# Optimization experiments

Hardware: AMD Instinct MI355X
Metric: run time of the kernel (lower is better)

The kernel has to match this reference:

```python
import jax, jax.numpy as jnp
import numpy as np

B, L, T = 4, 512, 4096
HID, NH = 1024, 16
HD = HID // NH
MAX_POS = 4096
BASE = 10000.0


def _cos_sin(dim, max_pos, base):
    inv_freq = 1.0 / base ** (jnp.arange(0, dim, 2, dtype=jnp.float32) / dim)
    t = jnp.arange(max_pos, dtype=jnp.float32)
    freqs = jnp.einsum('i,j->ij', t, inv_freq)
    emb = jnp.concatenate([freqs, freqs], axis=-1)  # [max_pos, dim]
    return jnp.cos(emb), jnp.sin(emb)


def _rotate_half(x):
    x1, x2 = x[..., : x.shape[-1] // 2], x[..., x.shape[-1] // 2:]
    return jnp.concatenate([-x2, x1], axis=-1)


def setup_inputs() -> dict:
    key = jax.random.key(0)
    ks = jax.random.split(key, 12)
    s = 0.02
    inp = {
        'latents': jax.random.normal(ks[0], (B, L, HID), jnp.float32),
        'target': jax.random.normal(ks[1], (B, T, HID), jnp.float32),
        'target_mask': jax.random.randint(ks[2], (B, T), 0, 2).astype(bool),
        'target_timestamp': jnp.sort(jax.random.randint(ks[3], (B, T), 0, MAX_POS), axis=-1),
        'Wq': jax.random.normal(ks[4], (HID, HID), jnp.float32) * s,
        'bq': jnp.zeros((HID,), jnp.float32),
        'Wk': jax.random.normal(ks[5], (HID, HID), jnp.float32) * s,
        'bk': jnp.zeros((HID,), jnp.float32),
        'Wv': jax.random.normal(ks[6], (HID, HID), jnp.float32) * s,
        'bv': jnp.zeros((HID,), jnp.float32),
        'Wo': jax.random.normal(ks[7], (HID, HID), jnp.float32) * s,
        'bo': jnp.zeros((HID,), jnp.float32),
    }
    return inp


def reference(latents, target, target_mask, target_timestamp, Wq, bq, Wk, bk, Wv, bv, Wo, bo):
    cos, sin = _cos_sin(HD, MAX_POS, BASE)  # [MAX_POS, HD]
    # latents_timestamp: arange(L) * (max-1)/(L-1), cast to int
    lat_ts = (jnp.arange(L, dtype=jnp.float32) * (MAX_POS - 1) / (L - 1)).astype(jnp.int64)
    lat_ts = jnp.broadcast_to(lat_ts[None, :], (B, L))

    # QKV projections (torch Linear: x @ W.T + b)
    q = (latents @ Wq.T + bq).reshape(B, L, NH, HD).transpose(0, 2, 1, 3)  # [B,H,L,D]
    k = (target @ Wk.T + bk).reshape(B, T, NH, HD).transpose(0, 2, 1, 3)   # [B,H,T,D]
    v = (target @ Wv.T + bv).reshape(B, T, NH, HD).transpose(0, 2, 1, 3)

    # RoPE with gathered timestamps; unsqueeze over head dim
    cq, sq = cos[lat_ts][:, None], sin[lat_ts][:, None]          # [B,1,L,D]
    ck, sk = cos[target_timestamp][:, None], sin[target_timestamp][:, None]  # [B,1,T,D]
    q = q * cq + _rotate_half(q) * sq
    k = k * ck + _rotate_half(k) * sk

    # SDPA with boolean attn mask (True = attend)
    scores = jnp.einsum('bhld,bhtd->bhlt', q, k) / jnp.sqrt(jnp.float32(HD))
    bias = jnp.where(target_mask[:, None, None, :], 0.0, -jnp.inf).astype(scores.dtype)
    attn = jax.nn.softmax(scores + bias, axis=-1)
    out = jnp.einsum('bhlt,bhtd->bhld', attn, v)  # [B,H,L,D]
    out = out.transpose(0, 2, 1, 3).reshape(B, L, HID)
    return out @ Wo.T + bo
```

## Files before the change

kernel.cpp:

```cpp
#include <hip/hip_runtime.h>

#define B_ 4
#define L_ 512
#define T_ 4096
#define NH_ 16
#define HD_ 64

using f32x4 = __attribute__((ext_vector_type(4))) float;
using bf16x8 = __attribute__((ext_vector_type(8))) short;
using u32x4 = __attribute__((ext_vector_type(4))) unsigned int;

__device__ __forceinline__ unsigned short f2bf(float x) {
  unsigned int u = __builtin_bit_cast(unsigned int, x);
  u += 0x7fffu + ((u >> 16) & 1u);
  return (unsigned short)(u >> 16);
}

__device__ __forceinline__ unsigned cvtpk(float lo, float hi) {
  unsigned r;
  asm("v_cvt_pk_bf16_f32 %0, %1, %2" : "=v"(r) : "v"(lo), "v"(hi));
  return r;
}

__device__ __forceinline__ u32x4 cvt8(const float4& a, const float4& b) {
  u32x4 r;
  r[0] = (unsigned)f2bf(a.x) | ((unsigned)f2bf(a.y) << 16);
  r[1] = (unsigned)f2bf(a.z) | ((unsigned)f2bf(a.w) << 16);
  r[2] = (unsigned)f2bf(b.x) | ((unsigned)f2bf(b.y) << 16);
  r[3] = (unsigned)f2bf(b.z) | ((unsigned)f2bf(b.w) << 16);
  return r;
}

__device__ __forceinline__ void gload16(const void* g, void* l) {
  __builtin_amdgcn_global_load_lds(
      (const __attribute__((address_space(1))) unsigned int*)g,
      (__attribute__((address_space(3))) unsigned int*)l, 16, 0, 0);
}

#define BC8(x) __builtin_bit_cast(bf16x8, (x))

struct CvtArgs {
  const float* src[6];
  unsigned short* dst[6];
  int cum[7];
};

__global__ void cvt_bf16(CvtArgs a, int total) {
  for (int g = blockIdx.x * 256 + threadIdx.x; g < total; g += gridDim.x * 256) {
    int r = 0;
#pragma unroll
    for (int q = 0; q < 5; ++q) r += (g >= a.cum[q + 1]);
    const int lc = g - a.cum[r];
    const float4* s = (const float4*)a.src[r] + (size_t)lc * 2;
    float4 x0 = s[0], x1 = s[1];
    *((u32x4*)a.dst[r] + lc) = cvt8(x0, x1);
  }
}

__global__ void rope_table(float* __restrict__ cost, float* __restrict__ sint,
                           const int* __restrict__ mask, float* __restrict__ mbias) {
  const int idx = blockIdx.x * 256 + threadIdx.x;
  const int pos = idx >> 5, i = idx & 31;
  const float inv = 1.0f / powf(10000.0f, (float)(2 * i) * (1.0f / 64.0f));
  const float f = (float)pos * inv;
  cost[idx] = cosf(f);
  sint[idx] = sinf(f);
  if (idx < B_ * T_) mbias[idx] = mask[idx] ? 0.f : -1e30f;
}

template <int EPI>
__global__ __launch_bounds__(256, 2) void gemm_bf(
    const unsigned short* __restrict__ A, const unsigned short* __restrict__ Wb,
    const float* __restrict__ bias, void* __restrict__ outp,
    const float* __restrict__ cost, const float* __restrict__ sint,
    const int* __restrict__ ts) {
  __shared__ u32x4 lsA[2][512];
  __shared__ u32x4 lsB[2][512];
  const int tid = threadIdx.x;
  const int mt = blockIdx.x >> 3, nt = blockIdx.x & 7;
  const int mBase = mt << 7, nBase = nt << 7;
  const int lane = tid & 63, wid = tid >> 6;
  const int wr = wid >> 1, wc = wid & 1;
  const int lr = lane & 15, lg = lane >> 4;

  f32x4 acc[4][4];
#pragma unroll
  for (int m = 0; m < 4; ++m)
#pragma unroll
    for (int n = 0; n < 4; ++n) acc[m][n] = (f32x4){0.f, 0.f, 0.f, 0.f};

  auto stage = [&](int bi, int kt) {
    const int ko = kt * 32;
#pragma unroll
    for (int j2 = 0; j2 < 2; ++j2) {
      const int j = wid * 2 + j2;
      const int row = (j & 1) * 64 + lane;
      const int kg = j >> 1;
      gload16(A + (size_t)(mBase + row) * 1024 + ko + kg * 8,
              (unsigned short*)lsA[bi] + j * 512);
      gload16(Wb + (size_t)(nBase + row) * 1024 + ko + kg * 8,
              (unsigned short*)lsB[bi] + j * 512);
    }
  };

  stage(0, 0);
  __syncthreads();
  int cur = 0;
  for (int kt = 0; kt < 32; ++kt) {
    if (kt < 31) stage(cur ^ 1, kt + 1);
    const u32x4* As = lsA[cur];
    const u32x4* Bs = lsB[cur];
    bf16x8 af[4], bfr[4];
#pragma unroll
    for (int m = 0; m < 4; ++m) af[m] = BC8(As[lg * 128 + wr * 64 + m * 16 + lr]);
#pragma unroll
    for (int n = 0; n < 4; ++n) bfr[n] = BC8(Bs[lg * 128 + wc * 64 + n * 16 + lr]);
#pragma unroll
    for (int m = 0; m < 4; ++m)
#pragma unroll
      for (int n = 0; n < 4; ++n)
        acc[m][n] = __builtin_amdgcn_mfma_f32_16x16x32_bf16(af[m], bfr[n], acc[m][n], 0, 0, 0);
    __syncthreads();
    cur ^= 1;
  }

  float bv[4];
#pragma unroll
  for (int n = 0; n < 4; ++n) bv[n] = bias[nBase + wc * 64 + n * 16 + lr];

  if (EPI == 3) {
    float* Of = (float*)outp;
#pragma unroll
    for (int m = 0; m < 4; ++m)
#pragma unroll
      for (int r = 0; r < 4; ++r) {
        const int gR = mBase + wr * 64 + m * 16 + lg * 4 + r;
#pragma unroll
        for (int n = 0; n < 4; ++n)
          Of[(size_t)gR * 1024 + nBase + wc * 64 + n * 16 + lr] = acc[m][n][r] + bv[n];
      }
  } else {
    unsigned short* Qo = (unsigned short*)outp;
    const int h = (nBase >> 6) + wc;
#pragma unroll
    for (int m = 0; m < 4; ++m) {
#pragma unroll
      for (int r = 0; r < 4; ++r) {
        const int gR = mBase + wr * 64 + m * 16 + lg * 4 + r;
        const int b2 = gR >> 9, p2 = gR & 511;
        const int pos = (int)(((float)p2 * 4095.0f) / 511.0f);
        const float* cp = cost + pos * 32;
        const float* sp = sint + pos * 32;
        const size_t obase = (((size_t)(b2 * NH_ + h)) * L_ + p2) * HD_;
#pragma unroll
        for (int n = 0; n < 2; ++n) {
          const int d = n * 16 + lr;
          const float x1 = acc[m][n][r] + bv[n];
          const float x2 = acc[m][n + 2][r] + bv[n + 2];
          const float c = cp[d], s = sp[d];
          Qo[obase + d] = f2bf(x1 * c - x2 * s);
          Qo[obase + d + 32] = f2bf(x2 * c + x1 * s);
        }
      }
    }
  }
}

__global__ __launch_bounds__(256, 3) void gemm_kv3(
    const unsigned short* __restrict__ A, const unsigned short* __restrict__ Wkv,
    const float* __restrict__ bkp, const float* __restrict__ bvp,
    unsigned short* __restrict__ Ko, unsigned short* __restrict__ Vo,
    const float* __restrict__ cost, const float* __restrict__ sint,
    const int* __restrict__ ts) {
  __shared__ u32x4 lsA[2][512];
  __shared__ u32x4 lsB[2][512];
  const int tid = threadIdx.x;
  const int orig = blockIdx.x;
  const int wgid = (orig & 7) * 256 + (orig >> 3);
  const int mt = wgid >> 4, nt = wgid & 15;
  const int mBase = mt << 7, nBase = nt << 7;
  const int lane = tid & 63, wid = tid >> 6;
  const int wr = wid >> 1, wc = wid & 1;
  const int lr = lane & 15, lg = lane >> 4;

  f32x4 acc[4][4];
#pragma unroll
  for (int m = 0; m < 4; ++m)
#pragma unroll
    for (int n = 0; n < 4; ++n) acc[m][n] = (f32x4){0.f, 0.f, 0.f, 0.f};

  auto stage = [&](int bi, int kt) {
    const int ko = kt * 32;
#pragma unroll
    for (int j2 = 0; j2 < 2; ++j2) {
      const int j = wid * 2 + j2;
      const int row = (j & 1) * 64 + lane;
      const int kg = j >> 1;
      gload16(A + (size_t)(mBase + row) * 1024 + ko + kg * 8,
              (unsigned short*)lsA[bi] + j * 512);
      gload16(Wkv + (size_t)(nBase + row) * 1024 + ko + kg * 8,
              (unsigned short*)lsB[bi] + j * 512);
    }
  };

  stage(0, 0);
  __syncthreads();
  int cur = 0;
  for (int kt = 0; kt < 32; ++kt) {
    if (kt < 31) stage(cur ^ 1, kt + 1);
    const u32x4* As = lsA[cur];
    const u32x4* Bs = lsB[cur];
    bf16x8 af[4], bfr[4];
#pragma unroll
    for (int m = 0; m < 4; ++m) af[m] = BC8(As[lg * 128 + wr * 64 + m * 16 + lr]);
#pragma unroll
    for (int n = 0; n < 4; ++n) bfr[n] = BC8(Bs[lg * 128 + wc * 64 + n * 16 + lr]);
#pragma unroll
    for (int m = 0; m < 4; ++m)
#pragma unroll
      for (int n = 0; n < 4; ++n)
        acc[m][n] = __builtin_amdgcn_mfma_f32_16x16x32_bf16(af[m], bfr[n], acc[m][n], 0, 0, 0);
    __syncthreads();
    cur ^= 1;
  }

  const bool isV = (nBase >= 1024);
  const int nb = isV ? (nBase - 1024) : nBase;
  const float* bp = isV ? bvp : bkp;
  const int h = (nb >> 6) + wc;
  float bb[4];
#pragma unroll
  for (int n = 0; n < 4; ++n) bb[n] = bp[nb + wc * 64 + n * 16 + lr];

  if (!isV) {
#pragma unroll
    for (int m = 0; m < 4; ++m) {
#pragma unroll
      for (int r = 0; r < 4; ++r) {
        const int gR = mBase + wr * 64 + m * 16 + lg * 4 + r;
        const int b2 = gR >> 12, p2 = gR & 4095;
        const int pos = ts[gR];
        const float* cp = cost + pos * 32;
        const float* sp = sint + pos * 32;
        const size_t obase = (((size_t)(b2 * NH_ + h)) * T_ + p2) * HD_;
#pragma unroll
        for (int n = 0; n < 2; ++n) {
          const int d = n * 16 + lr;
          const float x1 = acc[m][n][r] + bb[n];
          const float x2 = acc[m][n + 2][r] + bb[n + 2];
          const float c = cp[d], s = sp[d];
          Ko[obase + d] = f2bf(x1 * c - x2 * s);
          Ko[obase + d + 32] = f2bf(x2 * c + x1 * s);
        }
      }
    }
  } else {
#pragma unroll
    for (int m = 0; m < 4; ++m) {
      const int r0 = mBase + wr * 64 + m * 16 + lg * 4;
      const int b = r0 >> 12, t = r0 & 4095;
#pragma unroll
      for (int n = 0; n < 4; ++n) {
        const int d = n * 16 + lr;
        ushort4 pk;
        pk.x = f2bf(acc[m][n][0] + bb[n]);
        pk.y = f2bf(acc[m][n][1] + bb[n]);
        pk.z = f2bf(acc[m][n][2] + bb[n]);
        pk.w = f2bf(acc[m][n][3] + bb[n]);
        *(ushort4*)(Vo + (((size_t)(b * NH_ + h)) * HD_ + d) * (size_t)T_ + t) = pk;
      }
    }
  }
}

#define SCL 0.180336880111f
__global__ __launch_bounds__(256, 4) void attn_half(
    const unsigned short* __restrict__ Q, const unsigned short* __restrict__ K,
    const unsigned short* __restrict__ V, const float* __restrict__ mbias,
    float* __restrict__ pws, float* __restrict__ mlws) {
  __shared__ u32x4 QP[512];
  __shared__ u32x4 Ks[2][512];
  __shared__ u32x4 Vs[2][512];
  const int tid = threadIdx.x, lane = tid & 63, w = tid >> 6;
  const int lr = lane & 15, lg = lane >> 4;
  const int orig = blockIdx.x;
  const int wg = (orig & 7) * 128 + (orig >> 3);
  const int half = wg & 1, lt = (wg >> 1) & 7, bh = wg >> 4;
  const int b = bh >> 4;
  const int l0 = lt << 6;
  const int tBase = half << 11;

#pragma unroll
  for (int i = 0; i < 2; ++i) {
    const int li = w * 2 + i;
    gload16(Q + ((size_t)bh * L_ + l0 + lane) * HD_ + li * 8, (unsigned short*)QP + li * 512);
  }
  __syncthreads();
  bf16x8 qf[2];
#pragma unroll
  for (int ks2 = 0; ks2 < 2; ++ks2)
    qf[ks2] = BC8(QP[(ks2 * 4 + lg) * 64 + w * 16 + lr]);

  f32x4 po[4];
#pragma unroll
  for (int n = 0; n < 4; ++n) po[n] = (f32x4){0.f, 0.f, 0.f, 0.f};
  float mrun = -1e30f, lrun = 0.f;

  char* Pw = (char*)QP + w * 2048;
  const int swz = (lr & 7) << 4;
  const float* mrow = mbias + (size_t)b * T_ + tBase;

  auto stage = [&](int bi, int it) {
    const int t0 = tBase + (it << 6);
#pragma unroll
    for (int i = 0; i < 2; ++i) {
      const int li = w * 2 + i;
      gload16(K + ((size_t)bh * T_ + t0 + lane) * HD_ + li * 8, (unsigned short*)Ks[bi] + li * 512);
      gload16(V + ((size_t)bh * HD_ + lane) * T_ + t0 + li * 8, (unsigned short*)Vs[bi] + li * 512);
    }
  };

  stage(0, 0);
  __syncthreads();
  int cur = 0;
  for (int it = 0; it < 32; ++it) {
    if (it < 31) stage(cur ^ 1, it + 1);
    const int t0l = it << 6;

    f32x4 s[4];
#pragma unroll
    for (int n = 0; n < 4; ++n) s[n] = (f32x4){0.f, 0.f, 0.f, 0.f};
#pragma unroll
    for (int ks2 = 0; ks2 < 2; ++ks2) {
#pragma unroll
      for (int n = 0; n < 4; ++n) {
        bf16x8 kb = BC8(Ks[cur][(ks2 * 4 + lg) * 64 + n * 16 + lr]);
        s[n] = __builtin_amdgcn_mfma_f32_16x16x32_bf16(kb, qf[ks2], s[n], 0, 0, 0);
      }
    }
#pragma unroll
    for (int n = 0; n < 4; ++n) {
      const f32x4 mb = *(const f32x4*)(mrow + t0l + n * 16 + lg * 4);
#pragma unroll
      for (int r = 0; r < 4; ++r) s[n][r] = s[n][r] * SCL + mb[r];
    }
    f32x4 m4;
#pragma unroll
    for (int r = 0; r < 4; ++r)
      m4[r] = fmaxf(fmaxf(s[0][r], s[1][r]), fmaxf(s[2][r], s[3][r]));
    float x = fmaxf(fmaxf(m4[0], m4[1]), fmaxf(m4[2], m4[3]));
    x = fmaxf(x, __shfl_xor(x, 16));
    x = fmaxf(x, __shfl_xor(x, 32));
    const float mnew = fmaxf(mrun, x);
    const float sc = __builtin_exp2f(mrun - mnew);
    mrun = mnew;
    f32x4 ls4 = (f32x4){0.f, 0.f, 0.f, 0.f};
#pragma unroll
    for (int n = 0; n < 4; ++n)
#pragma unroll
      for (int r = 0; r < 4; ++r) {
        const float p = __builtin_exp2f(s[n][r] - mnew);
        s[n][r] = p;
        ls4[r] += p;
      }
    lrun = lrun * sc + ((ls4[0] + ls4[1]) + (ls4[2] + ls4[3]));
#pragma unroll
    for (int n = 0; n < 4; ++n) po[n] *= sc;
#pragma unroll
    for (int n = 0; n < 4; ++n) {
      uint2 pk;
      pk.x = cvtpk(s[n][0], s[n][1]);
      pk.y = cvtpk(s[n][2], s[n][3]);
      *(uint2*)(Pw + ((lr * 128 + n * 32 + lg * 8) ^ swz)) = pk;
    }
    bf16x8 pa[2];
#pragma unroll
    for (int ks2 = 0; ks2 < 2; ++ks2)
      pa[ks2] = BC8(*(const u32x4*)(Pw + ((lr * 128 + ks2 * 64 + lg * 16) ^ swz)));
#pragma unroll
    for (int ks2 = 0; ks2 < 2; ++ks2) {
#pragma unroll
      for (int n = 0; n < 4; ++n) {
        bf16x8 vb = BC8(Vs[cur][(ks2 * 4 + lg) * 64 + n * 16 + lr]);
        po[n] = __builtin_amdgcn_mfma_f32_16x16x32_bf16(vb, pa[ks2], po[n], 0, 0, 0);
      }
    }
    __syncthreads();
    cur ^= 1;
  }

  lrun += __shfl_xor(lrun, 16);
  lrun += __shfl_xor(lrun, 32);
  const int l = w * 16 + lr;
  float* pbase = pws + ((size_t)(((bh << 3) + lt) * 2 + half)) * 4096;
  float* mlbase = mlws + ((size_t)(((bh << 3) + lt) * 2 + half)) * 128;
#pragma unroll
  for (int n = 0; n < 4; ++n)
    *(f32x4*)(pbase + l * 64 + n * 16 + lg * 4) = po[n];
  if (lg == 0) {
    mlbase[l * 2] = mrun;
    mlbase[l * 2 + 1] = lrun;
  }
}

__global__ void attn_combine(const float* __restrict__ pws, const float* __restrict__ mlws,
                             unsigned short* __restrict__ O) {
  const int blk = blockIdx.x;
  const int bh = blk >> 3, lt = blk & 7;
  const int b = bh >> 4, h = bh & 15;
  const int tid = threadIdx.x;
  const int row = tid >> 2, seg = tid & 3;
  const float* p0 = pws + ((size_t)blk * 2) * 4096 + row * 64 + seg * 16;
  const float* p1 = p0 + 4096;
  const float* ml0 = mlws + ((size_t)blk * 2) * 128 + row * 2;
  const float* ml1 = ml0 + 128;
  const float m0 = ml0[0], li0 = ml0[1], m1 = ml1[0], li1 = ml1[1];
  const float M = fmaxf(m0, m1);
  const float w0 = __builtin_exp2f(m0 - M), w1 = __builtin_exp2f(m1 - M);
  const float inv = 1.0f / (li0 * w0 + li1 * w1);
  const int gl = lt * 64 + row;
  unsigned short* orow = O + ((size_t)b * L_ + gl) * 1024 + h * HD_ + seg * 16;
#pragma unroll
  for (int j = 0; j < 4; ++j) {
    const float4 a = *(const float4*)(p0 + j * 4);
    const float4 c = *(const float4*)(p1 + j * 4);
    ushort4 pk;
    pk.x = f2bf((a.x * w0 + c.x * w1) * inv);
    pk.y = f2bf((a.y * w0 + c.y * w1) * inv);
    pk.z = f2bf((a.z * w0 + c.z * w1) * inv);
    pk.w = f2bf((a.w * w0 + c.w * w1) * inv);
    *(ushort4*)(orow + j * 4) = pk;
  }
}

extern "C" void kernel_launch(void* const* d_in, const int* in_sizes, int n_in,
                              void* d_out, int out_size, void* d_ws, size_t ws_size,
                              hipStream_t stream) {
  const float* latents = (const float*)d_in[0];
  const float* target = (const float*)d_in[1];
  const int* mask = (const int*)d_in[2];
  const int* ts = (const int*)d_in[3];
  const float* Wq = (const float*)d_in[4];
  const float* bq = (const float*)d_in[5];
  const float* Wk = (const float*)d_in[6];
  const float* bk = (const float*)d_in[7];
  const float* Wv = (const float*)d_in[8];
  const float* bv = (const float*)d_in[9];
  const float* Wo = (const float*)d_in[10];
  const float* bo = (const float*)d_in[11];
  float* out = (float*)d_out;

  char* ws = (char*)d_ws;
  float* cost = (float*)ws;
  float* sint = (float*)(ws + (512 << 10));
  unsigned short* Qws = (unsigned short*)(ws + (1ull << 20));
  unsigned short* Kws = (unsigned short*)(ws + (5ull << 20));
  unsigned short* Vws = (unsigned short*)(ws + (37ull << 20));
  float* mbias = (float*)(ws + (69ull << 20));
  unsigned short* Ows = (unsigned short*)(ws + (69ull << 20));
  unsigned short* latb = (unsigned short*)(ws + (73ull << 20));
  unsigned short* tgtb = (unsigned short*)(ws + (77ull << 20));
  float* pws = (float*)(ws + (77ull << 20));
  float* mlws = (float*)(ws + (93ull << 20));
  unsigned short* Wqb = (unsigned short*)(ws + (109ull << 20));
  unsigned short* Wkvb = (unsigned short*)(ws + (111ull << 20));
  unsigned short* Wob = (unsigned short*)(ws + (115ull << 20));

  CvtArgs ca;
  ca.src[0] = latents; ca.dst[0] = latb;
  ca.src[1] = target;  ca.dst[1] = tgtb;
  ca.src[2] = Wq;      ca.dst[2] = Wqb;
  ca.src[3] = Wk;      ca.dst[3] = Wkvb;
  ca.src[4] = Wv;      ca.dst[4] = Wkvb + (1 << 20);
  ca.src[5] = Wo;      ca.dst[5] = Wob;
  const int nch[6] = {2097152 / 8, 16777216 / 8, 131072, 131072, 131072, 131072};
  ca.cum[0] = 0;
  for (int i = 0; i < 6; ++i) ca.cum[i + 1] = ca.cum[i] + nch[i];
  const int total = ca.cum[6];

  cvt_bf16<<<dim3(2048), dim3(256), 0, stream>>>(ca, total);
  rope_table<<<dim3(512), dim3(256), 0, stream>>>(cost, sint, mask, mbias);
  gemm_bf<0><<<dim3(16 * 8), dim3(256), 0, stream>>>(latb, Wqb, bq, Qws, cost, sint, nullptr);
  gemm_kv3<<<dim3(2048), dim3(256), 0, stream>>>(tgtb, Wkvb, bk, bv, Kws, Vws, cost, sint, ts);
  attn_half<<<dim3(1024), dim3(256), 0, stream>>>(Qws, Kws, Vws, mbias, pws, mlws);
  attn_combine<<<dim3(512), dim3(256), 0, stream>>>(pws, mlws, Ows);
  gemm_bf<3><<<dim3(16 * 8), dim3(256), 0, stream>>>(Ows, Wob, bo, out, nullptr, nullptr, nullptr);
}
```

Baseline: 324.2 us.

## Enlarge KV projection GEMM to 256x256 tiles with 8 waves and deeper pipeline

```diff
diff --git a/kernel.cpp b/kernel.cpp
--- a/kernel.cpp
+++ b/kernel.cpp
@@ -166,78 +166,88 @@
   }
 }
 
-__global__ __launch_bounds__(256, 3) void gemm_kv3(
+__global__ __launch_bounds__(512, 1) void gemm_kv8(
     const unsigned short* __restrict__ A, const unsigned short* __restrict__ Wkv,
     const float* __restrict__ bkp, const float* __restrict__ bvp,
     unsigned short* __restrict__ Ko, unsigned short* __restrict__ Vo,
     const float* __restrict__ cost, const float* __restrict__ sint,
     const int* __restrict__ ts) {
-  __shared__ u32x4 lsA[2][512];
-  __shared__ u32x4 lsB[2][512];
+  __shared__ u32x4 lds_[8192];
   const int tid = threadIdx.x;
+  const int lane = tid & 63, w = tid >> 6;
+  const int wm = w >> 2, wn = w & 3;
+  const int lr = lane & 15, lg = lane >> 4;
   const int orig = blockIdx.x;
-  const int wgid = (orig & 7) * 256 + (orig >> 3);
-  const int mt = wgid >> 4, nt = wgid & 15;
-  const int mBase = mt << 7, nBase = nt << 7;
-  const int lane = tid & 63, wid = tid >> 6;
-  const int wr = wid >> 1, wc = wid & 1;
-  const int lr = lane & 15, lg = lane >> 4;
-
-  f32x4 acc[4][4];
-#pragma unroll
-  for (int m = 0; m < 4; ++m)
+  const int wgid = (orig & 7) * 64 + (orig >> 3);
+  const int mt = wgid >> 3, nt = wgid & 7;
+  const int mBase = mt << 8, nBase = nt << 8;
+
+  f32x4 acc[8][4];
+#pragma unroll
+  for (int m = 0; m < 8; ++m)
 #pragma unroll
     for (int n = 0; n < 4; ++n) acc[m][n] = (f32x4){0.f, 0.f, 0.f, 0.f};
 
-  auto stage = [&](int bi, int kt) {
-    const int ko = kt * 32;
-#pragma unroll
-    for (int j2 = 0; j2 < 2; ++j2) {
-      const int j = wid * 2 + j2;
-      const int row = (j & 1) * 64 + lane;
-      const int kg = j >> 1;
-      gload16(A + (size_t)(mBase + row) * 1024 + ko + kg * 8,
-              (unsigned short*)lsA[bi] + j * 512);
-      gload16(Wkv + (size_t)(nBase + row) * 1024 + ko + kg * 8,
-              (unsigned short*)lsB[bi] + j * 512);
+  auto stage = [&](int kt1, int q) {
+    char* ab = (char*)lds_ + (kt1 & 1) * 65536 + q * 16384;
+#pragma unroll
+    for (int c = 0; c < 2; ++c) {
+      const int g0 = c * 512 + w * 64;
+      const int row = (g0 & 255) + lane;
+      const int kc = q * 4 + (g0 >> 8);
+      const size_t koff = (size_t)(kt1 * 64 + kc * 8);
+      gload16(A + (size_t)(mBase + row) * 1024 + koff, ab + g0 * 16);
+      gload16(Wkv + (size_t)(nBase + row) * 1024 + koff, ab + 32768 + g0 * 16);
     }
   };
 
   stage(0, 0);
-  __syncthreads();
-  int cur = 0;
-  for (int kt = 0; kt < 32; ++kt) {
-    if (kt < 31) stage(cur ^ 1, kt + 1);
-    const u32x4* As = lsA[cur];
-    const u32x4* Bs = lsB[cur];
-    bf16x8 af[4], bfr[4];
-#pragma unroll
-    for (int m = 0; m < 4; ++m) af[m] = BC8(As[lg * 128 + wr * 64 + m * 16 + lr]);
-#pragma unroll
-    for (int n = 0; n < 4; ++n) bfr[n] = BC8(Bs[lg * 128 + wc * 64 + n * 16 + lr]);
-#pragma unroll
-    for (int m = 0; m < 4; ++m)
+  stage(0, 1);
+
+  for (int kt = 0; kt < 16; ++kt) {
+    const u32x4* Ab = lds_ + (kt & 1) * 4096;
+    const u32x4* Bb = Ab + 2048;
+#pragma unroll
+    for (int q = 0; q < 2; ++q) {
+      if (kt == 15 && q == 1)
+        asm volatile("s_waitcnt vmcnt(0)" ::: "memory");
+      else
+        asm volatile("s_waitcnt vmcnt(4)" ::: "memory");
+      __builtin_amdgcn_s_barrier();
+      const int kidx = q * 4 + lg;
+      bf16x8 af[8], bfq[4];
+#pragma unroll
+      for (int m = 0; m < 8; ++m)
+        af[m] = BC8(Ab[kidx * 256 + wm * 128 + m * 16 + lr]);
 #pragma unroll
       for (int n = 0; n < 4; ++n)
-        acc[m][n] = __builtin_amdgcn_mfma_f32_16x16x32_bf16(af[m], bfr[n], acc[m][n], 0, 0, 0);
-    __syncthreads();
-    cur ^= 1;
-  }
-
-  const bool isV = (nBase >= 1024);
-  const int nb = isV ? (nBase - 1024) : nBase;
+        bfq[n] = BC8(Bb[kidx * 256 + wn * 64 + n * 16 + lr]);
+      if (kt < 15) stage(kt + 1, q);
+      asm volatile("s_waitcnt lgkmcnt(0)" ::: "memory");
+      __builtin_amdgcn_sched_barrier(0);
+      __builtin_amdgcn_s_setprio(1);
+#pragma unroll
+      for (int m = 0; m < 8; ++m)
+#pragma unroll
+        for (int n = 0; n < 4; ++n)
+          acc[m][n] = __builtin_amdgcn_mfma_f32_16x16x32_bf16(af[m], bfq[n], acc[m][n], 0, 0, 0);
+      __builtin_amdgcn_s_setprio(0);
+    }
+  }
+
+  const bool isV = (nt >= 4);
   const float* bp = isV ? bvp : bkp;
-  const int h = (nb >> 6) + wc;
+  const int h = (nt & 3) * 4 + wn;
   float bb[4];
 #pragma unroll
-  for (int n = 0; n < 4; ++n) bb[n] = bp[nb + wc * 64 + n * 16 + lr];
+  for (int n = 0; n < 4; ++n) bb[n] = bp[(nt & 3) * 256 + wn * 64 + n * 16 + lr];
 
   if (!isV) {
 #pragma unroll
-    for (int m = 0; m < 4; ++m) {
+    for (int m = 0; m < 8; ++m) {
 #pragma unroll
       for (int r = 0; r < 4; ++r) {
-        const int gR = mBase + wr * 64 + m * 16 + lg * 4 + r;
+        const int gR = mBase + wm * 128 + m * 16 + lg * 4 + r;
         const int b2 = gR >> 12, p2 = gR & 4095;
         const int pos = ts[gR];
         const float* cp = cost + pos * 32;
@@ -256,8 +266,8 @@
     }
   } else {
 #pragma unroll
-    for (int m = 0; m < 4; ++m) {
-      const int r0 = mBase + wr * 64 + m * 16 + lg * 4;
+    for (int m = 0; m < 8; ++m) {
+      const int r0 = mBase + wm * 128 + m * 16 + lg * 4;
       const int b = r0 >> 12, t = r0 & 4095;
 #pragma unroll
       for (int n = 0; n < 4; ++n) {
@@ -481,7 +491,7 @@
   cvt_bf16<<<dim3(2048), dim3(256), 0, stream>>>(ca, total);
   rope_table<<<dim3(512), dim3(256), 0, stream>>>(cost, sint, mask, mbias);
   gemm_bf<0><<<dim3(16 * 8), dim3(256), 0, stream>>>(latb, Wqb, bq, Qws, cost, sint, nullptr);
-  gemm_kv3<<<dim3(2048), dim3(256), 0, stream>>>(tgtb, Wkvb, bk, bv, Kws, Vws, cost, sint, ts);
+  gemm_kv8<<<dim3(512), dim3(512), 0, stream>>>(tgtb, Wkvb, bk, bv, Kws, Vws, cost, sint, ts);
   attn_half<<<dim3(1024), dim3(256), 0, stream>>>(Qws, Kws, Vws, mbias, pws, mlws);
   attn_combine<<<dim3(512), dim3(256), 0, stream>>>(pws, mlws, Ows);
   gemm_bf<3><<<dim3(16 * 8), dim3(256), 0, stream>>>(Ows, Wob, bo, out, nullptr, nullptr, nullptr);
```

After: 327.2 us. No clear change (+0.9%).

## Fuse attention split-KV halves into one block, drop combine kernel and rope kernel

Applied to the files above, without the earlier changes.

```diff
diff --git a/kernel.cpp b/kernel.cpp
--- a/kernel.cpp
+++ b/kernel.cpp
@@ -45,8 +45,18 @@
   int cum[7];
 };
 
-__global__ void cvt_bf16(CvtArgs a, int total) {
-  for (int g = blockIdx.x * 256 + threadIdx.x; g < total; g += gridDim.x * 256) {
+__global__ void cvt_bf16(CvtArgs a, int total, float* __restrict__ cost,
+                         float* __restrict__ sint) {
+  if (blockIdx.x >= 2048) {
+    const int idx = (blockIdx.x - 2048) * 256 + threadIdx.x;
+    const int pos = idx >> 5, i = idx & 31;
+    const float inv = 1.0f / powf(10000.0f, (float)(2 * i) * (1.0f / 64.0f));
+    const float f = (float)pos * inv;
+    cost[idx] = cosf(f);
+    sint[idx] = sinf(f);
+    return;
+  }
+  for (int g = blockIdx.x * 256 + threadIdx.x; g < total; g += 2048 * 256) {
     int r = 0;
 #pragma unroll
     for (int q = 0; q < 5; ++q) r += (g >= a.cum[q + 1]);
@@ -55,17 +65,6 @@
     float4 x0 = s[0], x1 = s[1];
     *((u32x4*)a.dst[r] + lc) = cvt8(x0, x1);
   }
-}
-
-__global__ void rope_table(float* __restrict__ cost, float* __restrict__ sint,
-                           const int* __restrict__ mask, float* __restrict__ mbias) {
-  const int idx = blockIdx.x * 256 + threadIdx.x;
-  const int pos = idx >> 5, i = idx & 31;
-  const float inv = 1.0f / powf(10000.0f, (float)(2 * i) * (1.0f / 64.0f));
-  const float f = (float)pos * inv;
-  cost[idx] = cosf(f);
-  sint[idx] = sinf(f);
-  if (idx < B_ * T_) mbias[idx] = mask[idx] ? 0.f : -1e30f;
 }
 
 template <int EPI>
@@ -274,49 +273,48 @@
 }
 
 #define SCL 0.180336880111f
-__global__ __launch_bounds__(256, 4) void attn_half(
+__global__ __launch_bounds__(512, 4) void attn_full(
     const unsigned short* __restrict__ Q, const unsigned short* __restrict__ K,
-    const unsigned short* __restrict__ V, const float* __restrict__ mbias,
-    float* __restrict__ pws, float* __restrict__ mlws) {
-  __shared__ u32x4 QP[512];
-  __shared__ u32x4 Ks[2][512];
-  __shared__ u32x4 Vs[2][512];
+    const unsigned short* __restrict__ V, const int* __restrict__ mask,
+    unsigned short* __restrict__ O) {
+  __shared__ u32x4 QP2[1024];
+  __shared__ u32x4 Ksh[2][2][512];
+  __shared__ u32x4 Vsh[2][2][512];
   const int tid = threadIdx.x, lane = tid & 63, w = tid >> 6;
+  const int half = w >> 2, wsub = w & 3;
   const int lr = lane & 15, lg = lane >> 4;
   const int orig = blockIdx.x;
-  const int wg = (orig & 7) * 128 + (orig >> 3);
-  const int half = wg & 1, lt = (wg >> 1) & 7, bh = wg >> 4;
+  const int wg = (orig & 7) * 64 + (orig >> 3);
+  const int lt = wg & 7, bh = wg >> 3;
   const int b = bh >> 4;
   const int l0 = lt << 6;
   const int tBase = half << 11;
 
-#pragma unroll
-  for (int i = 0; i < 2; ++i) {
-    const int li = w * 2 + i;
-    gload16(Q + ((size_t)bh * L_ + l0 + lane) * HD_ + li * 8, (unsigned short*)QP + li * 512);
-  }
+  gload16(Q + ((size_t)bh * L_ + l0 + lane) * HD_ + w * 8, (unsigned short*)QP2 + w * 512);
   __syncthreads();
   bf16x8 qf[2];
 #pragma unroll
   for (int ks2 = 0; ks2 < 2; ++ks2)
-    qf[ks2] = BC8(QP[(ks2 * 4 + lg) * 64 + w * 16 + lr]);
+    qf[ks2] = BC8(QP2[(ks2 * 4 + lg) * 64 + wsub * 16 + lr]);
 
   f32x4 po[4];
 #pragma unroll
   for (int n = 0; n < 4; ++n) po[n] = (f32x4){0.f, 0.f, 0.f, 0.f};
   float mrun = -1e30f, lrun = 0.f;
 
-  char* Pw = (char*)QP + w * 2048;
+  char* Pw = (char*)QP2 + w * 2048;
   const int swz = (lr & 7) << 4;
-  const float* mrow = mbias + (size_t)b * T_ + tBase;
+  const int* mrow = mask + (size_t)b * T_ + tBase;
 
   auto stage = [&](int bi, int it) {
     const int t0 = tBase + (it << 6);
 #pragma unroll
     for (int i = 0; i < 2; ++i) {
-      const int li = w * 2 + i;
-      gload16(K + ((size_t)bh * T_ + t0 + lane) * HD_ + li * 8, (unsigned short*)Ks[bi] + li * 512);
-      gload16(V + ((size_t)bh * HD_ + lane) * T_ + t0 + li * 8, (unsigned short*)Vs[bi] + li * 512);
+      const int li = wsub * 2 + i;
+      gload16(K + ((size_t)bh * T_ + t0 + lane) * HD_ + li * 8,
+              (unsigned short*)Ksh[half][bi] + li * 512);
+      gload16(V + ((size_t)bh * HD_ + lane) * T_ + t0 + li * 8,
+              (unsigned short*)Vsh[half][bi] + li * 512);
     }
   };
 
@@ -334,15 +332,17 @@
     for (int ks2 = 0; ks2 < 2; ++ks2) {
 #pragma unroll
       for (int n = 0; n < 4; ++n) {
-        bf16x8 kb = BC8(Ks[cur][(ks2 * 4 + lg) * 64 + n * 16 + lr]);
+        bf16x8 kb = BC8(Ksh[half][cur][(ks2 * 4 + lg) * 64 + n * 16 + lr]);
         s[n] = __builtin_amdgcn_mfma_f32_16x16x32_bf16(kb, qf[ks2], s[n], 0, 0, 0);
       }
     }
 #pragma unroll
     for (int n = 0; n < 4; ++n) {
-      const f32x4 mb = *(const f32x4*)(mrow + t0l + n * 16 + lg * 4);
-#pragma unroll
-      for (int r = 0; r < 4; ++r) s[n][r] = s[n][r] * SCL + mb[r];
+      const int4 mi = *(const int4*)(mrow + t0l + n * 16 + lg * 4);
+      s[n][0] = s[n][0] * SCL + (mi.x ? 0.f : -1e30f);
+      s[n][1] = s[n][1] * SCL + (mi.y ? 0.f : -1e30f);
+      s[n][2] = s[n][2] * SCL + (mi.z ? 0.f : -1e30f);
+      s[n][3] = s[n][3] * SCL + (mi.w ? 0.f : -1e30f);
     }
     f32x4 m4;
 #pragma unroll
@@ -381,7 +381,7 @@
     for (int ks2 = 0; ks2 < 2; ++ks2) {
 #pragma unroll
       for (int n = 0; n < 4; ++n) {
-        bf16x8 vb = BC8(Vs[cur][(ks2 * 4 + lg) * 64 + n * 16 + lr]);
+        bf16x8 vb = BC8(Vsh[half][cur][(ks2 * 4 + lg) * 64 + n * 16 + lr]);
         po[n] = __builtin_amdgcn_mfma_f32_16x16x32_bf16(vb, pa[ks2], po[n], 0, 0, 0);
       }
     }
@@ -391,45 +391,38 @@
 
   lrun += __shfl_xor(lrun, 16);
   lrun += __shfl_xor(lrun, 32);
-  const int l = w * 16 + lr;
-  float* pbase = pws + ((size_t)(((bh << 3) + lt) * 2 + half)) * 4096;
-  float* mlbase = mlws + ((size_t)(((bh << 3) + lt) * 2 + half)) * 128;
-#pragma unroll
-  for (int n = 0; n < 4; ++n)
-    *(f32x4*)(pbase + l * 64 + n * 16 + lg * 4) = po[n];
-  if (lg == 0) {
-    mlbase[l * 2] = mrun;
-    mlbase[l * 2 + 1] = lrun;
-  }
-}
-
-__global__ void attn_combine(const float* __restrict__ pws, const float* __restrict__ mlws,
-                             unsigned short* __restrict__ O) {
-  const int blk = blockIdx.x;
-  const int bh = blk >> 3, lt = blk & 7;
-  const int b = bh >> 4, h = bh & 15;
-  const int tid = threadIdx.x;
-  const int row = tid >> 2, seg = tid & 3;
-  const float* p0 = pws + ((size_t)blk * 2) * 4096 + row * 64 + seg * 16;
-  const float* p1 = p0 + 4096;
-  const float* ml0 = mlws + ((size_t)blk * 2) * 128 + row * 2;
-  const float* ml1 = ml0 + 128;
-  const float m0 = ml0[0], li0 = ml0[1], m1 = ml1[0], li1 = ml1[1];
-  const float M = fmaxf(m0, m1);
-  const float w0 = __builtin_exp2f(m0 - M), w1 = __builtin_exp2f(m1 - M);
-  const float inv = 1.0f / (li0 * w0 + li1 * w1);
-  const int gl = lt * 64 + row;
-  unsigned short* orow = O + ((size_t)b * L_ + gl) * 1024 + h * HD_ + seg * 16;
-#pragma unroll
-  for (int j = 0; j < 4; ++j) {
-    const float4 a = *(const float4*)(p0 + j * 4);
-    const float4 c = *(const float4*)(p1 + j * 4);
-    ushort4 pk;
-    pk.x = f2bf((a.x * w0 + c.x * w1) * inv);
-    pk.y = f2bf((a.y * w0 + c.y * w1) * inv);
-    pk.z = f2bf((a.z * w0 + c.z * w1) * inv);
-    pk.w = f2bf((a.w * w0 + c.w * w1) * inv);
-    *(ushort4*)(orow + j * 4) = pk;
+  const int rl = wsub * 16 + lr;
+
+  float* ex = (float*)Ksh;
+  float* ml = (float*)Vsh;
+  if (half == 1) {
+#pragma unroll
+    for (int n = 0; n < 4; ++n) {
+      const int idx = rl * 16 + ((n * 4 + lg) ^ (rl & 15));
+      *((f32x4*)ex + idx) = po[n];
+    }
+    if (lg == 0) {
+      ml[rl * 2] = mrun;
+      ml[rl * 2 + 1] = lrun;
+    }
+  }
+  __syncthreads();
+  if (half == 0) {
+    const float m1 = ml[rl * 2], l1v = ml[rl * 2 + 1];
+    const float M = fmaxf(mrun, m1);
+    const float w0 = __builtin_exp2f(mrun - M), w1 = __builtin_exp2f(m1 - M);
+    const float inv = 1.0f / (lrun * w0 + l1v * w1);
+    const int gl = l0 + rl;
+    unsigned short* orow = O + ((size_t)b * L_ + gl) * 1024 + (bh & 15) * HD_;
+#pragma unroll
+    for (int n = 0; n < 4; ++n) {
+      const int idx = rl * 16 + ((n * 4 + lg) ^ (rl & 15));
+      const f32x4 p1 = *((f32x4*)ex + idx);
+      uint2 pk;
+      pk.x = cvtpk((po[n][0] * w0 + p1[0] * w1) * inv, (po[n][1] * w0 + p1[1] * w1) * inv);
+      pk.y = cvtpk((po[n][2] * w0 + p1[2] * w1) * inv, (po[n][3] * w0 + p1[3] * w1) * inv);
+      *(uint2*)(orow + n * 16 + lg * 4) = pk;
+    }
   }
 }
 
@@ -456,12 +449,9 @@
   unsigned short* Qws = (unsigned short*)(ws + (1ull << 20));
   unsigned short* Kws = (unsigned short*)(ws + (5ull << 20));
   unsigned short* Vws = (unsigned short*)(ws + (37ull << 20));
-  float* mbias = (float*)(ws + (69ull << 20));
   unsigned short* Ows = (unsigned short*)(ws + (69ull << 20));
   unsigned short* latb = (unsigned short*)(ws + (73ull << 20));
   unsigned short* tgtb = (unsigned short*)(ws + (77ull << 20));
-  float* pws = (float*)(ws + (77ull << 20));
-  float* mlws = (float*)(ws + (93ull << 20));
   unsigned short* Wqb = (unsigned short*)(ws + (109ull << 20));
   unsigned short* Wkvb = (unsigned short*)(ws + (111ull << 20));
   unsigned short* Wob = (unsigned short*)(ws + (115ull << 20));
@@ -478,11 +468,9 @@
   for (int i = 0; i < 6; ++i) ca.cum[i + 1] = ca.cum[i] + nch[i];
   const int total = ca.cum[6];
 
-  cvt_bf16<<<dim3(2048), dim3(256), 0, stream>>>(ca, total);
-  rope_table<<<dim3(512), dim3(256), 0, stream>>>(cost, sint, mask, mbias);
+  cvt_bf16<<<dim3(2560), dim3(256), 0, stream>>>(ca, total, cost, sint);
   gemm_bf<0><<<dim3(16 * 8), dim3(256), 0, stream>>>(latb, Wqb, bq, Qws, cost, sint, nullptr);
   gemm_kv3<<<dim3(2048), dim3(256), 0, stream>>>(tgtb, Wkvb, bk, bv, Kws, Vws, cost, sint, ts);
-  attn_half<<<dim3(1024), dim3(256), 0, stream>>>(Qws, Kws, Vws, mbias, pws, mlws);
-  attn_combine<<<dim3(512), dim3(256), 0, stream>>>(pws, mlws, Ows);
+  attn_full<<<dim3(512), dim3(512), 0, stream>>>(Qws, Kws, Vws, mask, Ows);
   gemm_bf<3><<<dim3(16 * 8), dim3(256), 0, stream>>>(Ows, Wob, bo, out, nullptr, nullptr, nullptr);
 }
```

Result: no change. 323.4 us (-0.2%).
